# Kernel optimization log

Hardware: AMD Instinct MI355X
Metric: run time of the kernel (lower is better)

The kernel has to match this reference:

```python
import jax, jax.numpy as jnp
import numpy as np
from jax import lax

B_, H_, W_, DM = 4, 56, 56, 96
DI = int(2.0 * DM)          # d_inner = 192
NS = 16                     # d_state
RK = int(np.ceil(DM / 16))  # dt_rank = 6
KG = 4                      # scan directions
EPS = 1e-5


def setup_inputs() -> dict:
    key = jax.random.key(0)
    ks = jax.random.split(key, 10)
    x = jax.random.normal(ks[0], (B_, H_, W_, DM), jnp.float32)
    in_proj_w = jax.random.normal(ks[1], (2 * DI, DM), jnp.float32) * (1.0 / np.sqrt(DM))
    conv_w = jax.random.normal(ks[2], (DI, 1, 3, 3), jnp.float32) * (1.0 / 3.0)
    conv_b = jax.random.normal(ks[3], (DI,), jnp.float32) * 0.02
    x_proj_weight = jax.random.normal(ks[4], (KG, RK + 2 * NS, DI), jnp.float32) * (1.0 / np.sqrt(DI))
    dt_projs_weight = jax.random.normal(ks[5], (KG, DI, RK), jnp.float32) * (1.0 / np.sqrt(RK))
    dt_projs_bias = jax.random.uniform(ks[6], (KG, DI), jnp.float32, -4.0, -2.0)  # softplus -> small dt
    A_logs = jnp.tile(jnp.log(jnp.arange(1, NS + 1, dtype=jnp.float32))[None, :], (KG * DI, 1))
    Ds = jnp.ones((KG * DI,), jnp.float32)
    ln_w = jnp.ones((DI,), jnp.float32)
    ln_b = jnp.zeros((DI,), jnp.float32)
    out_proj_w = jax.random.normal(ks[7], (DM, DI), jnp.float32) * (1.0 / np.sqrt(DI))
    return dict(x=x, in_proj_w=in_proj_w, conv_w=conv_w, conv_b=conv_b,
                x_proj_weight=x_proj_weight, dt_projs_weight=dt_projs_weight,
                dt_projs_bias=dt_projs_bias, A_logs=A_logs, Ds=Ds,
                ln_w=ln_w, ln_b=ln_b, out_proj_w=out_proj_w)


def selective_scan(u, delta, A, Bm, Cm, Dv, delta_bias):
    # u, delta: [B,K,D,L]; A: [K,D,N]; Bm, Cm: [B,K,N,L]; Dv, delta_bias: [K,D]
    delta = jax.nn.softplus(delta + delta_bias[None, :, :, None])
    u_l = jnp.moveaxis(u, -1, 0)      # [L,B,K,D]
    d_l = jnp.moveaxis(delta, -1, 0)  # [L,B,K,D]
    B_l = jnp.moveaxis(Bm, -1, 0)     # [L,B,K,N]
    C_l = jnp.moveaxis(Cm, -1, 0)     # [L,B,K,N]
    N = A.shape[-1]
    h0 = jnp.zeros(u.shape[:3] + (N,), u.dtype)  # [B,K,D,N]

    def step(h, inp):
        u_t, d_t, b_t, c_t = inp
        dA = jnp.exp(d_t[..., None] * A)                       # [B,K,D,N]
        h = dA * h + (d_t * u_t)[..., None] * b_t[:, :, None, :]
        y = jnp.einsum('bkdn,bkn->bkd', h, c_t)
        return h, y

    _, ys = lax.scan(step, h0, (u_l, d_l, B_l, C_l))           # ys: [L,B,K,D]
    return jnp.moveaxis(ys, 0, -1) + u * Dv[None, :, :, None]  # [B,K,D,L]


def forward(x, in_proj_w, conv_w, conv_b, x_proj_weight, dt_projs_weight,
            dt_projs_bias, A_logs, Ds, ln_w, ln_b, out_proj_w):
    B, H, W, _ = x.shape
    Di = conv_w.shape[0]
    L = H * W
    xz = x @ in_proj_w.T                       # [B,H,W,2*Di]
    xx, z = jnp.split(xz, 2, axis=-1)
    z = jax.nn.silu(z)
    xc = jnp.transpose(xx, (0, 3, 1, 2))       # [B,Di,H,W]
    xc = lax.conv_general_dilated(xc, conv_w, (1, 1), ((1, 1), (1, 1)),
                                  feature_group_count=Di,
                                  dimension_numbers=('NCHW', 'OIHW', 'NCHW'))
    xc = jax.nn.silu(xc + conv_b[None, :, None, None])
    # cross-scan: identity, transpose(HW), and their flips
    x_flat = xc.reshape(B, Di, L)
    x_wh = jnp.transpose(xc, (0, 1, 3, 2)).reshape(B, Di, L)
    x_hwwh = jnp.stack([x_flat, x_wh], axis=1)                       # [B,2,Di,L]
    xs = jnp.concatenate([x_hwwh, jnp.flip(x_hwwh, axis=-1)], axis=1)  # [B,4,Di,L]
    x_dbl = jnp.einsum('bkdl,kcd->bkcl', xs, x_proj_weight)
    R = dt_projs_weight.shape[-1]
    N = A_logs.shape[-1]
    dts, Bs, Cs = jnp.split(x_dbl, [R, R + N], axis=2)               # [B,K,R,L],[B,K,N,L],[B,K,N,L]
    dts = jnp.einsum('bkrl,kdr->bkdl', dts, dt_projs_weight)         # [B,K,Di,L]
    A = -jnp.exp(A_logs).reshape(KG, Di, N)
    Dv = Ds.reshape(KG, Di)
    out_y = selective_scan(xs, dts, A, Bs, Cs, Dv, dt_projs_bias)    # [B,4,Di,L]
    # cross-merge
    inv_y = jnp.flip(out_y[:, 2:4], axis=-1)
    wh_y = jnp.transpose(out_y[:, 1].reshape(B, Di, W, H), (0, 1, 3, 2)).reshape(B, Di, L)
    invwh_y = jnp.transpose(inv_y[:, 1].reshape(B, Di, W, H), (0, 1, 3, 2)).reshape(B, Di, L)
    y = out_y[:, 0] + inv_y[:, 0] + wh_y + invwh_y                   # [B,Di,L]
    y = jnp.transpose(y, (0, 2, 1))                                  # [B,L,Di]
    mu = y.mean(-1, keepdims=True)
    var = ((y - mu) ** 2).mean(-1, keepdims=True)
    y = (y - mu) / jnp.sqrt(var + EPS) * ln_w + ln_b
    y = y.reshape(B, H, W, Di) * z
    return y @ out_proj_w.T                                          # [B,H,W,d_model]


def reference(x, in_proj_w, conv_w, conv_b, x_proj_weight, dt_projs_weight,
              dt_projs_bias, A_logs, Ds, ln_w, ln_b, out_proj_w):
    return forward(x, in_proj_w, conv_w, conv_b, x_proj_weight, dt_projs_weight,
                   dt_projs_bias, A_logs, Ds, ln_w, ln_b, out_proj_w)
```

## Files before the change

### kernel.cpp

```cpp
#include <hip/hip_runtime.h>
#include <hip/hip_bf16.h>
#include <math.h>

#define BB 4
#define HH 56
#define WW 56
#define DM 96
#define DI 192
#define NS 16
#define RK 6
#define KG 4
#define LL (HH*WW)
#define NPIX (BB*LL)
#define CHL 32
#define NCH (LL/CHL)
#define NDT (DI/16)
#define XP 32
#define NC 38
#define PAD 196
#define LNPX 8

static __device__ __forceinline__ int qmap(int k, int l){
    int m = (k & 2) ? (LL - 1 - l) : l;
    if (k & 1) { int w = m / HH; int h = m % HH; return h * WW + w; }
    return m;
}

static __device__ __forceinline__ float silu(float x){ return x / (1.f + __expf(-x)); }

__global__ __launch_bounds__(256) void k_prep(const float* __restrict__ Win,
    const float* __restrict__ Wout, const float* __restrict__ dtw,
    float* __restrict__ WinT, float* __restrict__ WoutT, float* __restrict__ dtwT)
{
    int t = blockIdx.x*256 + threadIdx.x;
    if (t < 384*DM){
        int i = t / 384, c = t % 384;
        WinT[t] = Win[(size_t)c*DM + i];
    } else if (t < 384*DM + DI*DM){
        int t2 = t - 384*DM;
        int i = t2 / DM, c = t2 % DM;
        WoutT[t2] = Wout[(size_t)c*DI + i];
    } else if (t < 384*DM + DI*DM + KG*RK*DI){
        int t2 = t - 384*DM - DI*DM;
        int k = t2 / (RK*DI);
        int r = (t2 % (RK*DI)) / DI;
        int d = t2 % DI;
        dtwT[t2] = dtw[((size_t)k*DI + d)*RK + r];
    }
}

__global__ __launch_bounds__(384) void k_inproj(const float* __restrict__ x,
        const float* __restrict__ WinT,
        float* __restrict__ conv_in, float* __restrict__ z_silu)
{
    __shared__ float sx[8*DM];
    int pb  = blockIdx.x * 8;
    int c = threadIdx.x;
    sx[c]       = x[(size_t)pb*DM + c];
    sx[c + 384] = x[(size_t)pb*DM + 384 + c];
    __syncthreads();
    float a0=0,a1=0,a2=0,a3=0,a4=0,a5=0,a6=0,a7=0;
    #pragma unroll 4
    for (int i = 0; i < DM; ++i){
        float w = WinT[(size_t)i*384 + c];
        a0=fmaf(sx[i],w,a0);        a1=fmaf(sx[DM+i],w,a1);
        a2=fmaf(sx[2*DM+i],w,a2);   a3=fmaf(sx[3*DM+i],w,a3);
        a4=fmaf(sx[4*DM+i],w,a4);   a5=fmaf(sx[5*DM+i],w,a5);
        a6=fmaf(sx[6*DM+i],w,a6);   a7=fmaf(sx[7*DM+i],w,a7);
    }
    if (c < DI){
        conv_in[(size_t)(pb+0)*DI+c]=a0; conv_in[(size_t)(pb+1)*DI+c]=a1;
        conv_in[(size_t)(pb+2)*DI+c]=a2; conv_in[(size_t)(pb+3)*DI+c]=a3;
        conv_in[(size_t)(pb+4)*DI+c]=a4; conv_in[(size_t)(pb+5)*DI+c]=a5;
        conv_in[(size_t)(pb+6)*DI+c]=a6; conv_in[(size_t)(pb+7)*DI+c]=a7;
    } else {
        int d = c - DI;
        z_silu[(size_t)(pb+0)*DI+d]=silu(a0); z_silu[(size_t)(pb+1)*DI+d]=silu(a1);
        z_silu[(size_t)(pb+2)*DI+d]=silu(a2); z_silu[(size_t)(pb+3)*DI+d]=silu(a3);
        z_silu[(size_t)(pb+4)*DI+d]=silu(a4); z_silu[(size_t)(pb+5)*DI+d]=silu(a5);
        z_silu[(size_t)(pb+6)*DI+d]=silu(a6); z_silu[(size_t)(pb+7)*DI+d]=silu(a7);
    }
}

__global__ __launch_bounds__(256) void k_conv(const float* __restrict__ conv_in,
    const float* __restrict__ cw, const float* __restrict__ cb,
    float* __restrict__ xc)
{
    __shared__ float scw[DI*9];
    int tid = threadIdx.x;
    for (int t = tid; t < DI*9; t += 256) scw[t] = cw[t];
    __syncthreads();
    int idx = blockIdx.x*256 + tid;
    int d = idx % DI;
    int p = (idx / DI) % LL;
    int b = idx / (DI*LL);
    int h = p / WW, w = p % WW;
    float acc = cb[d];
    #pragma unroll
    for (int dy = -1; dy <= 1; ++dy){
        int hy = h + dy; if (hy < 0 || hy >= HH) continue;
        #pragma unroll
        for (int dx = -1; dx <= 1; ++dx){
            int wx = w + dx; if (wx < 0 || wx >= WW) continue;
            acc = fmaf(conv_in[((size_t)b*LL + hy*WW + wx)*DI + d],
                       scw[d*9 + (dy+1)*3 + (dx+1)], acc);
        }
    }
    xc[idx] = silu(acc);
}

static __device__ __forceinline__ float dot4(float4 u, float4 w, float acc){
    acc = fmaf(u.x,w.x,acc); acc = fmaf(u.y,w.y,acc);
    acc = fmaf(u.z,w.z,acc); acc = fmaf(u.w,w.w,acc);
    return acc;
}

static __device__ __forceinline__ float mkdelta(const float* tr, const float* w,
                                                float bb){
    float a = bb;
    #pragma unroll
    for (int r = 0; r < RK; ++r) a = fmaf(tr[r], w[r], a);
    return (a > 20.f) ? a : __logf(1.f + __expf(a));
}

#define HSP(i, pw, comp) h[i] = fmaf(pw, h[i], dlu*(comp))
#define YS(i, comp) y = fmaf(h[i], (comp), y)

__global__ __launch_bounds__(192, 4) void k_xproj(const float* __restrict__ xc,
   const float* __restrict__ xpw, const float* __restrict__ dtb,
   const float* __restrict__ dtwT,
   float* __restrict__ dts, float* __restrict__ Bsb, float* __restrict__ Csb,
   float* __restrict__ hend, float* __restrict__ sumdl)
{
    __shared__ float su[XP*PAD];
    __shared__ float sxd[XP][40];
    int gb = blockIdx.x;
    int bk = gb / NCH, ch = gb % NCH;
    int b = bk >> 2, k = bk & 3;
    int l0 = ch*XP;
    int tid = threadIdx.x;

    for (int t = tid; t < XP*48; t += 192){
        int lo = t / 48, i4 = t % 48;
        int px = qmap(k, l0 + lo);
        float4 u = ((const float4*)(xc + ((size_t)b*LL + px)*DI))[i4];
        *((float4*)&su[lo*PAD + i4*4]) = u;
    }
    __syncthreads();

    for (int q = tid; q < 19*16; q += 192){
        int c2 = q >> 4, lo = q & 15;
        int c0 = 2*c2, c1 = c0 + 1;
        const float4* p0 = (const float4*)(xpw + ((size_t)k*NC + c0)*DI);
        const float4* p1 = (const float4*)(xpw + ((size_t)k*NC + c1)*DI);
        const float4* ua = (const float4*)&su[lo*PAD];
        const float4* ub = (const float4*)&su[(lo+16)*PAD];
        float a00=0,a01=0,a10=0,a11=0;
        #pragma unroll 4
        for (int i4 = 0; i4 < 48; ++i4){
            float4 u0 = ua[i4], u1 = ub[i4];
            float4 w0 = p0[i4], w1 = p1[i4];
            a00 = dot4(u0,w0,a00); a01 = dot4(u0,w1,a01);
            a10 = dot4(u1,w0,a10); a11 = dot4(u1,w1,a11);
        }
        sxd[lo][c0] = a00;    sxd[lo][c1] = a01;
        sxd[lo+16][c0] = a10; sxd[lo+16][c1] = a11;
    }
    __syncthreads();

    for (int t = tid; t < XP*NS; t += 192){
        int lo = t / NS, n = t % NS;
        Bsb[((size_t)bk*LL + l0+lo)*NS + n] = sxd[lo][RK + n];
        Csb[((size_t)bk*LL + l0+lo)*NS + n] = sxd[lo][RK + NS + n];
    }
    for (int t = tid; t < XP*RK; t += 192){
        int lo = t / RK, r = t % RK;
        dts[((size_t)bk*LL + l0+lo)*RK + r] = sxd[lo][r];
    }

    {
        int d = tid;
        float wdt[RK];
        {
            const float* wp = dtwT + (size_t)k*RK*DI + d;
            #pragma unroll
            for (int r = 0; r < RK; ++r) wdt[r] = wp[(size_t)r*DI];
        }
        float bb = dtb[k*DI + d];
        float h[NS];
        #pragma unroll
        for (int n = 0; n < NS; ++n) h[n] = 0.f;
        float S = 0.f;
        #pragma unroll 1
        for (int lo = 0; lo < XP; ++lo){
            float uu = su[lo*PAD + d];
            float dl = mkdelta(&sxd[lo][0], wdt, bb);
            S += dl;
            float dlu = dl * uu;
            float r   = __expf(-dl);
            float r2  = r*r,   r3  = r2*r,  r4  = r2*r2;
            float r5  = r4*r,  r6  = r4*r2, r7  = r4*r3,  r8  = r4*r4;
            float r9  = r8*r,  r10 = r8*r2, r11 = r8*r3,  r12 = r8*r4;
            float r13 = r8*r5, r14 = r8*r6, r15 = r8*r7,  r16 = r8*r8;
            const float* bv = &sxd[lo][RK];
            HSP(0, r,  bv[0]);  HSP(1, r2,  bv[1]);  HSP(2, r3,  bv[2]);  HSP(3, r4,  bv[3]);
            HSP(4, r5, bv[4]);  HSP(5, r6,  bv[5]);  HSP(6, r7,  bv[6]);  HSP(7, r8,  bv[7]);
            HSP(8, r9, bv[8]);  HSP(9, r10, bv[9]);  HSP(10, r11, bv[10]); HSP(11, r12, bv[11]);
            HSP(12, r13, bv[12]); HSP(13, r14, bv[13]); HSP(14, r15, bv[14]); HSP(15, r16, bv[15]);
        }
        size_t hb = ((size_t)bk*NCH + ch)*NS*DI + d;
        #pragma unroll
        for (int n = 0; n < NS; ++n) hend[hb + (size_t)n*DI] = h[n];
        sumdl[((size_t)bk*NCH + ch)*DI + d] = S;
    }
}

__global__ __launch_bounds__(256) void k_scan2(float* __restrict__ hend,
    const float* __restrict__ sumdl, const float* __restrict__ Alog)
{
    int blk = blockIdx.x;
    int bk = blk / NDT, part = blk % NDT;
    int k = bk & 3;
    int tid = threadIdx.x;
    int dsub = tid & 15, n = tid >> 4;
    int d = part*16 + dsub;
    float An = -__expf(Alog[((size_t)k*DI + d)*NS + n]);
    size_t base  = ((size_t)bk*NCH)*NS*DI + (size_t)n*DI + d;
    size_t sbase = (size_t)bk*NCH*DI + d;
    float H = 0.f;
    float he0 = hend[base], S0 = sumdl[sbase];
    float he1 = hend[base + (size_t)NS*DI], S1 = sumdl[sbase + DI];
    for (int c = 0; c < NCH; ++c){
        float heN = 0.f, SN = 0.f;
        if (c+2 < NCH){
            heN = hend [base  + (size_t)(c+2)*NS*DI];
            SN  = sumdl[sbase + (size_t)(c+2)*DI];
        }
        hend[base + (size_t)c*NS*DI] = H;
        H  = fmaf(__expf(An*S0), H, he0);
        he0 = he1; S0 = S1;
        he1 = heN; S1 = SN;
    }
}

__global__ __launch_bounds__(192, 6) void k_scan3(const float* __restrict__ dts,
    const float* __restrict__ xc, const float* __restrict__ Bsb,
    const float* __restrict__ Csb,
    const float* __restrict__ dtb, const float* __restrict__ dtwT,
    const float* __restrict__ Dsv, const float* __restrict__ H0,
    float* __restrict__ ys)
{
    __shared__ float sB[CHL][NS], sC[CHL][NS];
    __shared__ float sT[CHL][RK];
    int bid = blockIdx.x;
    int bk = bid / NCH, ch = bid % NCH;
    int b = bk >> 2, k = bk & 3;
    int d = threadIdx.x;
    int l0 = ch*CHL;

    const float* xbase = xc + (size_t)b*LL*DI + d;
    const float* Bb = Bsb + ((size_t)bk*LL + l0)*NS;
    const float* Cb = Csb + ((size_t)bk*LL + l0)*NS;
    const float* Tb = dts + ((size_t)bk*LL + l0)*RK;
    float* ybase = ys + ((size_t)bk*LL + l0)*DI + d;
    for (int t = d; t < CHL*NS; t += 192){
        ((float*)sB)[t] = Bb[t];
        ((float*)sC)[t] = Cb[t];
    }
    for (int t = d; t < CHL*RK; t += 192) ((float*)sT)[t] = Tb[t];

    float wdt[RK];
    {
        const float* wp = dtwT + (size_t)k*RK*DI + d;
        #pragma unroll
        for (int r = 0; r < RK; ++r) wdt[r] = wp[(size_t)r*DI];
    }
    float bb = dtb[k*DI + d];
    float Dv = Dsv[k*DI + d];

    float h[NS];
    size_t hb = ((size_t)bk*NCH + ch)*NS*DI + d;
    #pragma unroll
    for (int n = 0; n < NS; ++n) h[n] = H0[hb + (size_t)n*DI];
    __syncthreads();

    float pu[2][4];
    #pragma unroll
    for (int j = 0; j < 4; ++j) pu[0][j] = xbase[(size_t)qmap(k, l0+j)*DI];
    #pragma unroll 1
    for (int g = 0; g < CHL/4; ++g){
        int cur = g & 1, nxt = cur ^ 1;
        if (g + 1 < CHL/4){
            #pragma unroll
            for (int j = 0; j < 4; ++j)
                pu[nxt][j] = xbase[(size_t)qmap(k, l0+(g+1)*4+j)*DI];
        }
        #pragma unroll
        for (int j = 0; j < 4; ++j){
            int l = g*4 + j;
            float uu = pu[cur][j];
            float dl = mkdelta(&sT[l][0], wdt, bb);
            float dlu = dl * uu;
            float r   = __expf(-dl);
            float r2  = r*r,   r3  = r2*r,  r4  = r2*r2;
            float r5  = r4*r,  r6  = r4*r2, r7  = r4*r3,  r8  = r4*r4;
            float r9  = r8*r,  r10 = r8*r2, r11 = r8*r3,  r12 = r8*r4;
            float r13 = r8*r5, r14 = r8*r6, r15 = r8*r7,  r16 = r8*r8;
            const float4* br = (const float4*)&sB[l][0];
            const float4* cr = (const float4*)&sC[l][0];
            float4 b0 = br[0], b1 = br[1], b2 = br[2], b3 = br[3];
            HSP(0, r,  b0.x);  HSP(1, r2,  b0.y);  HSP(2, r3,  b0.z);  HSP(3, r4,  b0.w);
            HSP(4, r5, b1.x);  HSP(5, r6,  b1.y);  HSP(6, r7,  b1.z);  HSP(7, r8,  b1.w);
            HSP(8, r9, b2.x);  HSP(9, r10, b2.y);  HSP(10, r11, b2.z); HSP(11, r12, b2.w);
            HSP(12, r13, b3.x); HSP(13, r14, b3.y); HSP(14, r15, b3.z); HSP(15, r16, b3.w);
            float4 c0 = cr[0], c1 = cr[1], c2 = cr[2], c3 = cr[3];
            float y = uu * Dv;
            YS(0,c0.x);  YS(1,c0.y);  YS(2,c0.z);  YS(3,c0.w);
            YS(4,c1.x);  YS(5,c1.y);  YS(6,c1.z);  YS(7,c1.w);
            YS(8,c2.x);  YS(9,c2.y);  YS(10,c2.z); YS(11,c2.w);
            YS(12,c3.x); YS(13,c3.y); YS(14,c3.z); YS(15,c3.w);
            ybase[(size_t)l*DI] = y;
        }
    }
}

__global__ __launch_bounds__(192) void k_lnout(const float* __restrict__ ys,
    const float* __restrict__ z_silu, const float* __restrict__ lnw,
    const float* __restrict__ lnb, const float* __restrict__ WoutT,
    float* __restrict__ out)
{
    __shared__ float syz[LNPX][DI];
    __shared__ float red_s[LNPX][3], red_q[LNPX][3];
    __shared__ float smu[LNPX], srs[LNPX];
    int pg0 = blockIdx.x * LNPX;
    int b = pg0 / LL, q0 = pg0 % LL;
    int tid = threadIdx.x;
    float wln = lnw[tid], bln = lnb[tid];
    float v[LNPX];
    #pragma unroll
    for (int px = 0; px < LNPX; ++px){
        int q = q0 + px;
        int hh = q / WW, w = q % WW;
        int l1 = w*HH + hh;
        const float* r0 = ys + (((size_t)(b*4+0)*LL) + q)*DI + tid;
        const float* r1 = ys + (((size_t)(b*4+1)*LL) + l1)*DI + tid;
        const float* r2 = ys + (((size_t)(b*4+2)*LL) + (LL-1-q))*DI + tid;
        const float* r3 = ys + (((size_t)(b*4+3)*LL) + (LL-1-l1))*DI + tid;
        v[px] = (*r0 + *r1) + (*r2 + *r3);
    }
    int wid = tid >> 6, lane = tid & 63;
    #pragma unroll
    for (int px = 0; px < LNPX; ++px){
        float s = v[px], sq = v[px]*v[px];
        #pragma unroll
        for (int m = 32; m >= 1; m >>= 1){ s += __shfl_xor(s,m); sq += __shfl_xor(sq,m); }
        if (lane == 0){ red_s[px][wid] = s; red_q[px][wid] = sq; }
    }
    __syncthreads();
    if (tid < LNPX){
        float ts = red_s[tid][0]+red_s[tid][1]+red_s[tid][2];
        float tq = red_q[tid][0]+red_q[tid][1]+red_q[tid][2];
        float mu = ts*(1.f/DI);
        float var = tq*(1.f/DI) - mu*mu;
        smu[tid] = mu; srs[tid] = rsqrtf(var + 1e-5f);
    }
    __syncthreads();
    #pragma unroll
    for (int px = 0; px < LNPX; ++px){
        float z = z_silu[(size_t)(pg0+px)*DI + tid];
        syz[px][tid] = ((v[px]-smu[px])*srs[px]*wln + bln) * z;
    }
    __syncthreads();
    int g = tid / DM, c = tid % DM;
    float a0=0,a1=0,a2=0,a3=0;
    #pragma unroll 4
    for (int i = 0; i < DI; ++i){
        float w = WoutT[(size_t)i*DM + c];
        a0 = fmaf(syz[g*4+0][i], w, a0);
        a1 = fmaf(syz[g*4+1][i], w, a1);
        a2 = fmaf(syz[g*4+2][i], w, a2);
        a3 = fmaf(syz[g*4+3][i], w, a3);
    }
    out[(size_t)(pg0+g*4+0)*DM + c] = a0;
    out[(size_t)(pg0+g*4+1)*DM + c] = a1;
    out[(size_t)(pg0+g*4+2)*DM + c] = a2;
    out[(size_t)(pg0+g*4+3)*DM + c] = a3;
}

extern "C" void kernel_launch(void* const* d_in, const int* in_sizes, int n_in,
                              void* d_out, int out_size, void* d_ws, size_t ws_size,
                              hipStream_t stream)
{
    const float* x    = (const float*)d_in[0];
    const float* Win  = (const float*)d_in[1];
    const float* cw   = (const float*)d_in[2];
    const float* cb   = (const float*)d_in[3];
    const float* xpw  = (const float*)d_in[4];
    const float* dtw  = (const float*)d_in[5];
    const float* dtb  = (const float*)d_in[6];
    const float* Alog = (const float*)d_in[7];
    const float* Dsv  = (const float*)d_in[8];
    const float* lnw  = (const float*)d_in[9];
    const float* lnb  = (const float*)d_in[10];
    const float* Wout = (const float*)d_in[11];
    float* out = (float*)d_out;

    float* ws      = (float*)d_ws;
    float* conv_in = ws;
    float* z_silu  = conv_in + (size_t)NPIX*DI;
    float* xc      = z_silu  + (size_t)NPIX*DI;
    float* ys      = xc      + (size_t)NPIX*DI;
    float* Bsb     = ys      + (size_t)BB*KG*LL*DI;
    float* Csb     = Bsb     + (size_t)BB*KG*LL*NS;
    float* sumdl   = Csb     + (size_t)BB*KG*LL*NS;
    float* dts     = sumdl   + (size_t)BB*KG*NCH*DI;
    float* WinT    = dts     + (size_t)BB*KG*LL*RK;
    float* WoutT   = WinT    + (size_t)DM*2*DI;
    float* dtwT    = WoutT   + (size_t)DI*DM;
    float* hend    = dtwT    + (size_t)KG*RK*DI;

    hipLaunchKernelGGL(k_prep,   dim3((384*DM + DI*DM + KG*RK*DI + 255)/256), dim3(256), 0, stream,
                       Win, Wout, dtw, WinT, WoutT, dtwT);
    hipLaunchKernelGGL(k_inproj, dim3(NPIX/8), dim3(384), 0, stream, x, WinT, conv_in, z_silu);
    hipLaunchKernelGGL(k_conv,   dim3((NPIX*DI)/256), dim3(256), 0, stream, conv_in, cw, cb, xc);
    hipLaunchKernelGGL(k_xproj,  dim3(BB*KG*NCH), dim3(192), 0, stream, xc, xpw, dtb, dtwT,
                       dts, Bsb, Csb, hend, sumdl);
    hipLaunchKernelGGL(k_scan2, dim3(BB*KG*NDT), dim3(256), 0, stream,
                       hend, sumdl, Alog);
    hipLaunchKernelGGL(k_scan3, dim3(BB*KG*NCH), dim3(192), 0, stream,
                       dts, xc, Bsb, Csb, dtb, dtwT, Dsv, hend, ys);
    hipLaunchKernelGGL(k_lnout,  dim3(NPIX/LNPX), dim3(192), 0, stream, ys, z_silu, lnw, lnb, WoutT, out);
}
```

Baseline: 271.8 us.

## Scatter scan outputs to spatial order and enlarge pixel tiles in projections

The scan kernel now writes each direction's output at the spatial pixel index from qmap, so the layernorm/out-projection kernel reads all four directions at the same contiguous pixel instead of gathering transposed and flipped rows. The in-projection tile grows from 8 to 16 pixels per block and the out-projection from 4 to 8 pixels per thread, so each weight load is reused across more pixels. The cost is more accumulator registers, which may lower occupancy, and half as many blocks for the two projection kernels.

Measured after the change: 286.4 us. +5.4%, slower.

```diff
diff --git a/kernel.cpp b/kernel.cpp
--- a/kernel.cpp
+++ b/kernel.cpp
@@ -18,7 +18,8 @@
 #define XP 32
 #define NC 38
 #define PAD 196
-#define LNPX 8
+#define LNPX 16
+#define IPX 16
 
 static __device__ __forceinline__ int qmap(int k, int l){
     int m = (k & 2) ? (LL - 1 - l) : l;
@@ -53,32 +54,27 @@
         const float* __restrict__ WinT,
         float* __restrict__ conv_in, float* __restrict__ z_silu)
 {
-    __shared__ float sx[8*DM];
-    int pb  = blockIdx.x * 8;
+    __shared__ float sx[IPX*DM];
+    int pb = blockIdx.x * IPX;
     int c = threadIdx.x;
-    sx[c]       = x[(size_t)pb*DM + c];
-    sx[c + 384] = x[(size_t)pb*DM + 384 + c];
-    __syncthreads();
-    float a0=0,a1=0,a2=0,a3=0,a4=0,a5=0,a6=0,a7=0;
+    for (int t = c; t < IPX*DM; t += 384) sx[t] = x[(size_t)pb*DM + t];
+    __syncthreads();
+    float a[IPX];
+    #pragma unroll
+    for (int p = 0; p < IPX; ++p) a[p] = 0.f;
     #pragma unroll 4
     for (int i = 0; i < DM; ++i){
         float w = WinT[(size_t)i*384 + c];
-        a0=fmaf(sx[i],w,a0);        a1=fmaf(sx[DM+i],w,a1);
-        a2=fmaf(sx[2*DM+i],w,a2);   a3=fmaf(sx[3*DM+i],w,a3);
-        a4=fmaf(sx[4*DM+i],w,a4);   a5=fmaf(sx[5*DM+i],w,a5);
-        a6=fmaf(sx[6*DM+i],w,a6);   a7=fmaf(sx[7*DM+i],w,a7);
+        #pragma unroll
+        for (int p = 0; p < IPX; ++p) a[p] = fmaf(sx[p*DM + i], w, a[p]);
     }
     if (c < DI){
-        conv_in[(size_t)(pb+0)*DI+c]=a0; conv_in[(size_t)(pb+1)*DI+c]=a1;
-        conv_in[(size_t)(pb+2)*DI+c]=a2; conv_in[(size_t)(pb+3)*DI+c]=a3;
-        conv_in[(size_t)(pb+4)*DI+c]=a4; conv_in[(size_t)(pb+5)*DI+c]=a5;
-        conv_in[(size_t)(pb+6)*DI+c]=a6; conv_in[(size_t)(pb+7)*DI+c]=a7;
+        #pragma unroll
+        for (int p = 0; p < IPX; ++p) conv_in[(size_t)(pb+p)*DI + c] = a[p];
     } else {
         int d = c - DI;
-        z_silu[(size_t)(pb+0)*DI+d]=silu(a0); z_silu[(size_t)(pb+1)*DI+d]=silu(a1);
-        z_silu[(size_t)(pb+2)*DI+d]=silu(a2); z_silu[(size_t)(pb+3)*DI+d]=silu(a3);
-        z_silu[(size_t)(pb+4)*DI+d]=silu(a4); z_silu[(size_t)(pb+5)*DI+d]=silu(a5);
-        z_silu[(size_t)(pb+6)*DI+d]=silu(a6); z_silu[(size_t)(pb+7)*DI+d]=silu(a7);
+        #pragma unroll
+        for (int p = 0; p < IPX; ++p) z_silu[(size_t)(pb+p)*DI + d] = silu(a[p]);
     }
 }
 
@@ -262,7 +258,7 @@
     const float* Bb = Bsb + ((size_t)bk*LL + l0)*NS;
     const float* Cb = Csb + ((size_t)bk*LL + l0)*NS;
     const float* Tb = dts + ((size_t)bk*LL + l0)*RK;
-    float* ybase = ys + ((size_t)bk*LL + l0)*DI + d;
+    float* ybase = ys + (size_t)bk*LL*DI + d;
     for (int t = d; t < CHL*NS; t += 192){
         ((float*)sB)[t] = Bb[t];
         ((float*)sC)[t] = Cb[t];
@@ -285,15 +281,21 @@
     __syncthreads();
 
     float pu[2][4];
-    #pragma unroll
-    for (int j = 0; j < 4; ++j) pu[0][j] = xbase[(size_t)qmap(k, l0+j)*DI];
+    int   pq[2][4];
+    #pragma unroll
+    for (int j = 0; j < 4; ++j){
+        pq[0][j] = qmap(k, l0+j);
+        pu[0][j] = xbase[(size_t)pq[0][j]*DI];
+    }
     #pragma unroll 1
     for (int g = 0; g < CHL/4; ++g){
         int cur = g & 1, nxt = cur ^ 1;
         if (g + 1 < CHL/4){
             #pragma unroll
-            for (int j = 0; j < 4; ++j)
-                pu[nxt][j] = xbase[(size_t)qmap(k, l0+(g+1)*4+j)*DI];
+            for (int j = 0; j < 4; ++j){
+                pq[nxt][j] = qmap(k, l0+(g+1)*4+j);
+                pu[nxt][j] = xbase[(size_t)pq[nxt][j]*DI];
+            }
         }
         #pragma unroll
         for (int j = 0; j < 4; ++j){
@@ -319,7 +321,7 @@
             YS(4,c1.x);  YS(5,c1.y);  YS(6,c1.z);  YS(7,c1.w);
             YS(8,c2.x);  YS(9,c2.y);  YS(10,c2.z); YS(11,c2.w);
             YS(12,c3.x); YS(13,c3.y); YS(14,c3.z); YS(15,c3.w);
-            ybase[(size_t)l*DI] = y;
+            ybase[(size_t)pq[cur][j]*DI] = y;
         }
     }
 }
@@ -339,13 +341,11 @@
     float v[LNPX];
     #pragma unroll
     for (int px = 0; px < LNPX; ++px){
-        int q = q0 + px;
-        int hh = q / WW, w = q % WW;
-        int l1 = w*HH + hh;
+        size_t q = q0 + px;
         const float* r0 = ys + (((size_t)(b*4+0)*LL) + q)*DI + tid;
-        const float* r1 = ys + (((size_t)(b*4+1)*LL) + l1)*DI + tid;
-        const float* r2 = ys + (((size_t)(b*4+2)*LL) + (LL-1-q))*DI + tid;
-        const float* r3 = ys + (((size_t)(b*4+3)*LL) + (LL-1-l1))*DI + tid;
+        const float* r1 = ys + (((size_t)(b*4+1)*LL) + q)*DI + tid;
+        const float* r2 = ys + (((size_t)(b*4+2)*LL) + q)*DI + tid;
+        const float* r3 = ys + (((size_t)(b*4+3)*LL) + q)*DI + tid;
         v[px] = (*r0 + *r1) + (*r2 + *r3);
     }
     int wid = tid >> 6, lane = tid & 63;
@@ -372,19 +372,18 @@
     }
     __syncthreads();
     int g = tid / DM, c = tid % DM;
-    float a0=0,a1=0,a2=0,a3=0;
+    float a[8];
+    #pragma unroll
+    for (int p = 0; p < 8; ++p) a[p] = 0.f;
     #pragma unroll 4
     for (int i = 0; i < DI; ++i){
         float w = WoutT[(size_t)i*DM + c];
-        a0 = fmaf(syz[g*4+0][i], w, a0);
-        a1 = fmaf(syz[g*4+1][i], w, a1);
-        a2 = fmaf(syz[g*4+2][i], w, a2);
-        a3 = fmaf(syz[g*4+3][i], w, a3);
-    }
-    out[(size_t)(pg0+g*4+0)*DM + c] = a0;
-    out[(size_t)(pg0+g*4+1)*DM + c] = a1;
-    out[(size_t)(pg0+g*4+2)*DM + c] = a2;
-    out[(size_t)(pg0+g*4+3)*DM + c] = a3;
+        #pragma unroll
+        for (int p = 0; p < 8; ++p) a[p] = fmaf(syz[g*8+p][i], w, a[p]);
+    }
+    #pragma unroll
+    for (int p = 0; p < 8; ++p)
+        out[(size_t)(pg0 + g*8 + p)*DM + c] = a[p];
 }
 
 extern "C" void kernel_launch(void* const* d_in, const int* in_sizes, int n_in,
@@ -421,7 +420,7 @@
 
     hipLaunchKernelGGL(k_prep,   dim3((384*DM + DI*DM + KG*RK*DI + 255)/256), dim3(256), 0, stream,
                        Win, Wout, dtw, WinT, WoutT, dtwT);
-    hipLaunchKernelGGL(k_inproj, dim3(NPIX/8), dim3(384), 0, stream, x, WinT, conv_in, z_silu);
+    hipLaunchKernelGGL(k_inproj, dim3(NPIX/IPX), dim3(384), 0, stream, x, WinT, conv_in, z_silu);
     hipLaunchKernelGGL(k_conv,   dim3((NPIX*DI)/256), dim3(256), 0, stream, conv_in, cw, cb, xc);
     hipLaunchKernelGGL(k_xproj,  dim3(BB*KG*NCH), dim3(192), 0, stream, xc, xpw, dtb, dtwT,
                        dts, Bsb, Csb, hend, sumdl);
```

## Scatter scan outputs to pixel order and widen x-projection blocks

Applied to the files above, without the earlier changes.

The scan kernel now writes each direction's output at the pixel index given by qmap instead of in scan order. This lets the LayerNorm/out-projection kernel read all four directions contiguously at the same pixel, removing its transposed and reversed gathers. Separately, k_xproj is launched with 320 threads so all 304 projection work items run in a single pass, and the state-recurrence part is guarded to the first 192 threads. The cost is scattered, strided writes in the scan kernel and idle threads during the recurrence phase of k_xproj.

After: 274.6 us. No clear change (+1.0%).

```diff
diff --git a/kernel.cpp b/kernel.cpp
--- a/kernel.cpp
+++ b/kernel.cpp
@@ -126,7 +126,7 @@
 #define HSP(i, pw, comp) h[i] = fmaf(pw, h[i], dlu*(comp))
 #define YS(i, comp) y = fmaf(h[i], (comp), y)
 
-__global__ __launch_bounds__(192, 4) void k_xproj(const float* __restrict__ xc,
+__global__ __launch_bounds__(320, 6) void k_xproj(const float* __restrict__ xc,
    const float* __restrict__ xpw, const float* __restrict__ dtb,
    const float* __restrict__ dtwT,
    float* __restrict__ dts, float* __restrict__ Bsb, float* __restrict__ Csb,
@@ -140,7 +140,7 @@
     int l0 = ch*XP;
     int tid = threadIdx.x;
 
-    for (int t = tid; t < XP*48; t += 192){
+    for (int t = tid; t < XP*48; t += 320){
         int lo = t / 48, i4 = t % 48;
         int px = qmap(k, l0 + lo);
         float4 u = ((const float4*)(xc + ((size_t)b*LL + px)*DI))[i4];
@@ -148,7 +148,8 @@
     }
     __syncthreads();
 
-    for (int q = tid; q < 19*16; q += 192){
+    if (tid < 19*16){
+        int q = tid;
         int c2 = q >> 4, lo = q & 15;
         int c0 = 2*c2, c1 = c0 + 1;
         const float4* p0 = (const float4*)(xpw + ((size_t)k*NC + c0)*DI);
@@ -168,17 +169,17 @@
     }
     __syncthreads();
 
-    for (int t = tid; t < XP*NS; t += 192){
+    for (int t = tid; t < XP*NS; t += 320){
         int lo = t / NS, n = t % NS;
         Bsb[((size_t)bk*LL + l0+lo)*NS + n] = sxd[lo][RK + n];
         Csb[((size_t)bk*LL + l0+lo)*NS + n] = sxd[lo][RK + NS + n];
     }
-    for (int t = tid; t < XP*RK; t += 192){
+    for (int t = tid; t < XP*RK; t += 320){
         int lo = t / RK, r = t % RK;
         dts[((size_t)bk*LL + l0+lo)*RK + r] = sxd[lo][r];
     }
 
-    {
+    if (tid < DI){
         int d = tid;
         float wdt[RK];
         {
@@ -262,7 +263,7 @@
     const float* Bb = Bsb + ((size_t)bk*LL + l0)*NS;
     const float* Cb = Csb + ((size_t)bk*LL + l0)*NS;
     const float* Tb = dts + ((size_t)bk*LL + l0)*RK;
-    float* ybase = ys + ((size_t)bk*LL + l0)*DI + d;
+    float* ybase = ys + (size_t)bk*LL*DI + d;
     for (int t = d; t < CHL*NS; t += 192){
         ((float*)sB)[t] = Bb[t];
         ((float*)sC)[t] = Cb[t];
@@ -285,15 +286,21 @@
     __syncthreads();
 
     float pu[2][4];
-    #pragma unroll
-    for (int j = 0; j < 4; ++j) pu[0][j] = xbase[(size_t)qmap(k, l0+j)*DI];
+    int   pq[2][4];
+    #pragma unroll
+    for (int j = 0; j < 4; ++j){
+        pq[0][j] = qmap(k, l0+j);
+        pu[0][j] = xbase[(size_t)pq[0][j]*DI];
+    }
     #pragma unroll 1
     for (int g = 0; g < CHL/4; ++g){
         int cur = g & 1, nxt = cur ^ 1;
         if (g + 1 < CHL/4){
             #pragma unroll
-            for (int j = 0; j < 4; ++j)
-                pu[nxt][j] = xbase[(size_t)qmap(k, l0+(g+1)*4+j)*DI];
+            for (int j = 0; j < 4; ++j){
+                pq[nxt][j] = qmap(k, l0+(g+1)*4+j);
+                pu[nxt][j] = xbase[(size_t)pq[nxt][j]*DI];
+            }
         }
         #pragma unroll
         for (int j = 0; j < 4; ++j){
@@ -319,7 +326,7 @@
             YS(4,c1.x);  YS(5,c1.y);  YS(6,c1.z);  YS(7,c1.w);
             YS(8,c2.x);  YS(9,c2.y);  YS(10,c2.z); YS(11,c2.w);
             YS(12,c3.x); YS(13,c3.y); YS(14,c3.z); YS(15,c3.w);
-            ybase[(size_t)l*DI] = y;
+            ybase[(size_t)pq[cur][j]*DI] = y;
         }
     }
 }
@@ -339,13 +346,11 @@
     float v[LNPX];
     #pragma unroll
     for (int px = 0; px < LNPX; ++px){
-        int q = q0 + px;
-        int hh = q / WW, w = q % WW;
-        int l1 = w*HH + hh;
+        size_t q = q0 + px;
         const float* r0 = ys + (((size_t)(b*4+0)*LL) + q)*DI + tid;
-        const float* r1 = ys + (((size_t)(b*4+1)*LL) + l1)*DI + tid;
-        const float* r2 = ys + (((size_t)(b*4+2)*LL) + (LL-1-q))*DI + tid;
-        const float* r3 = ys + (((size_t)(b*4+3)*LL) + (LL-1-l1))*DI + tid;
+        const float* r1 = ys + (((size_t)(b*4+1)*LL) + q)*DI + tid;
+        const float* r2 = ys + (((size_t)(b*4+2)*LL) + q)*DI + tid;
+        const float* r3 = ys + (((size_t)(b*4+3)*LL) + q)*DI + tid;
         v[px] = (*r0 + *r1) + (*r2 + *r3);
     }
     int wid = tid >> 6, lane = tid & 63;
@@ -423,7 +428,7 @@
                        Win, Wout, dtw, WinT, WoutT, dtwT);
     hipLaunchKernelGGL(k_inproj, dim3(NPIX/8), dim3(384), 0, stream, x, WinT, conv_in, z_silu);
     hipLaunchKernelGGL(k_conv,   dim3((NPIX*DI)/256), dim3(256), 0, stream, conv_in, cw, cb, xc);
-    hipLaunchKernelGGL(k_xproj,  dim3(BB*KG*NCH), dim3(192), 0, stream, xc, xpw, dtb, dtwT,
+    hipLaunchKernelGGL(k_xproj,  dim3(BB*KG*NCH), dim3(320), 0, stream, xc, xpw, dtb, dtwT,
                        dts, Bsb, Csb, hend, sumdl);
     hipLaunchKernelGGL(k_scan2, dim3(BB*KG*NDT), dim3(256), 0, stream,
                        hend, sumdl, Alog);
```
